# Kernel optimization log

Hardware: AMD Instinct MI355X
Metric: run time of the kernel (lower is better)

## Reference

```python
import jax, jax.numpy as jnp
import numpy as np

B, N_BOX, N_THING, ROI = 2, 32, 4, 28
H, W = 768, 704
N_STUFF = 6
N_CLS = N_STUFF + N_THING  # 10
NEG = -100.0


def setup_inputs() -> dict:
    key = jax.random.key(0)
    k1, k2, k3, k4 = jax.random.split(key, 4)
    sem_logits = jax.random.normal(k1, (B, N_CLS, H, W), jnp.float32)
    roi_msk_logits = jax.random.normal(k2, (B, N_BOX, N_THING, ROI, ROI), jnp.float32)
    cls = jax.random.randint(k3, (B, N_BOX), 0, N_THING, jnp.int32)
    u = jax.random.uniform(k4, (B, N_BOX, 4), jnp.float32)
    y0 = u[..., 0] * (H - 80.0)
    x0 = u[..., 1] * (W - 80.0)
    y1 = jnp.minimum(y0 + 32.0 + u[..., 2] * (H / 3.0), H - 1.0)
    x1 = jnp.minimum(x0 + 32.0 + u[..., 3] * (W / 3.0), W - 1.0)
    bbx = jnp.stack([y0, x0, y1, x1], axis=-1)  # (y_min, x_min, y_max, x_max)
    img_size = jnp.array([H, W], jnp.int32)
    return {"sem_logits": sem_logits, "roi_msk_logits": roi_msk_logits,
            "bbx": bbx, "cls": cls, "img_size": img_size}


def _bilinear_paste(msk, bbx, img_size, Hs, Ws):
    # msk: [B,N,R,R]; per-box bilinear resize (align_corners=False) to (h,w) and paste
    # into a [B,N,Hs,Ws] canvas filled with -100, clipped to the image.
    R = msk.shape[-1]
    ref = jnp.floor(bbx).astype(jnp.int32)  # torch .long()/int() truncation (boxes >= 0)
    y0, x0, y1, x1 = ref[..., 0], ref[..., 1], ref[..., 2], ref[..., 3]
    h = jnp.maximum(y1 - y0 + 1, 1).astype(jnp.float32)
    w = jnp.maximum(x1 - x0 + 1, 1).astype(jnp.float32)
    yy = jnp.arange(Hs, dtype=jnp.float32)[None, None, :]          # [1,1,H]
    sy = jnp.clip((yy - y0[..., None] + 0.5) * (R / h)[..., None] - 0.5, 0.0, R - 1.0)
    ylo = jnp.floor(sy).astype(jnp.int32)
    yhi = jnp.minimum(ylo + 1, R - 1)
    wy = sy - ylo                                                   # [B,N,H]
    xx = jnp.arange(Ws, dtype=jnp.float32)[None, None, :]
    sx = jnp.clip((xx - x0[..., None] + 0.5) * (R / w)[..., None] - 0.5, 0.0, R - 1.0)
    xlo = jnp.floor(sx).astype(jnp.int32)
    xhi = jnp.minimum(xlo + 1, R - 1)
    wx = sx - xlo                                                   # [B,N,W]
    rows = (jnp.take_along_axis(msk, ylo[..., None], axis=2) * (1.0 - wy[..., None])
            + jnp.take_along_axis(msk, yhi[..., None], axis=2) * wy[..., None])  # [B,N,H,R]
    up = (jnp.take_along_axis(rows, xlo[:, :, None, :], axis=3) * (1.0 - wx[:, :, None, :])
          + jnp.take_along_axis(rows, xhi[:, :, None, :], axis=3) * wx[:, :, None, :])  # [B,N,H,W]
    yi = jnp.arange(Hs, dtype=jnp.int32)[None, None, :]
    xi = jnp.arange(Ws, dtype=jnp.int32)[None, None, :]
    in_y = (yi >= jnp.maximum(y0, 0)[..., None]) & (yi < jnp.minimum(y1 + 1, img_size[0])[..., None])
    in_x = (xi >= jnp.maximum(x0, 0)[..., None]) & (xi < jnp.minimum(x1 + 1, img_size[1])[..., None])
    inside = in_y[..., :, None] & in_x[..., None, :]
    return jnp.where(inside, up, NEG)


def _fused_logits(sem_logits, roi_msk_logits, bbx, cls, img_size):
    Bs, _, Hs, Ws = sem_logits.shape
    Nb = cls.shape[1]
    # gather per-box mask logits for its predicted thing class: [B,N,R,R]
    msk = roi_msk_logits[jnp.arange(Bs)[:, None], jnp.arange(Nb)[None, :], cls]
    po_mask = _bilinear_paste(msk, bbx, img_size, Hs, Ws)          # [B,N,H,W]
    # semantic-logit crops per box (po_sem_stride = 1)
    iy0 = jnp.floor(bbx[..., 0]).astype(jnp.int32)
    ix0 = jnp.floor(bbx[..., 1]).astype(jnp.int32)
    iy1 = (jnp.round(bbx[..., 2]) + 1.0).astype(jnp.int32)
    ix1 = (jnp.round(bbx[..., 3]) + 1.0).astype(jnp.int32)
    yi = jnp.arange(Hs, dtype=jnp.int32)[None, None, :]
    xi = jnp.arange(Ws, dtype=jnp.int32)[None, None, :]
    in2 = (((yi >= iy0[..., None]) & (yi < iy1[..., None]))[..., :, None]
           & ((xi >= ix0[..., None]) & (xi < ix1[..., None]))[..., None, :])
    sem_sel = sem_logits[:, N_STUFF:][jnp.arange(Bs)[:, None], cls]  # [B,N,H,W]
    po_inst = jnp.where(in2, sem_sel, NEG)
    combined = (jax.nn.sigmoid(po_inst) + jax.nn.sigmoid(po_mask)) * (po_inst + po_mask)
    return jnp.concatenate([sem_logits[:, :N_STUFF], combined], axis=1)  # [B,6+N,H,W]


def _label_single(pp, sp, cl):
    # pp: panoptic argmax [H,W]; sp: semantic argmax [H,W]; cl: [N] thing classes
    Nb = cl.shape[0]
    is_inst = pp >= N_STUFF
    nmap = jnp.clip(pp - N_STUFF, 0, Nb - 1)
    # joint histogram counts[n, c] = #pixels with po_pred == 6+n and sem_pred == c
    key = jnp.where(is_inst, (pp - N_STUFF) * N_CLS + sp, Nb * N_CLS)
    counts = jnp.zeros(Nb * N_CLS + 1, jnp.int32).at[key.ravel()].add(1)[:Nb * N_CLS].reshape(Nb, N_CLS)
    present = counts.sum(1) > 0
    idx = jnp.cumsum(present.astype(jnp.int32)) - 1  # enumeration order of torch.unique ids
    maj = jnp.argmax(counts, axis=1).astype(jnp.int32)  # ties -> smallest class (matches unique+argmax)
    frac = counts.max(1).astype(jnp.float32) / jnp.maximum(counts.sum(1), 1).astype(jnp.float32)
    thing = cl.astype(jnp.int32) + N_STUFF
    match = maj == thing
    to_stuff = (~match) & (frac >= 0.5) & (maj < N_STUFF)
    sem_val = jnp.where(to_stuff, maj, thing)
    inst_val = jnp.where(to_stuff, -1, idx)
    po_sem = jnp.where(is_inst, sem_val[nmap], pp)
    po_inst = jnp.where(is_inst, inst_val[nmap], -1)
    # po_min_stuff_area = 0 (default) -> stuff-area filter is a no-op
    sh = jnp.zeros(N_STUFF + 1, jnp.int32).at[jnp.where(po_sem < N_STUFF, po_sem, N_STUFF).ravel()].add(1)[:N_STUFF]
    s_present = sh > 0
    s_rank = jnp.cumsum(s_present.astype(jnp.int32)) - 1
    n_stuff = s_present.astype(jnp.int32).sum()
    ih = jnp.zeros(Nb + 1, jnp.int32).at[jnp.where(po_inst >= 0, po_inst, Nb).ravel()].add(1)[:Nb]
    i_present = ih > 0
    i_rank = jnp.cumsum(i_present.astype(jnp.int32)) - 1
    seam = jnp.where((po_inst < 0) & (po_sem < N_STUFF),
                     1 + s_rank[jnp.clip(po_sem, 0, N_STUFF - 1)], 0)
    seam = jnp.where(po_inst >= 0, 1 + n_stuff + i_rank[jnp.clip(po_inst, 0, Nb - 1)], seam)
    L = 1 + N_STUFF + Nb  # fixed-size padded po_cls (torch version is variable-length)
    cls_out = jnp.full(L, 255, jnp.int32)
    cls_out = cls_out.at[jnp.where(s_present, 1 + s_rank, L)].set(
        jnp.arange(N_STUFF, dtype=jnp.int32), mode='drop')
    inst_sem = jnp.full(Nb, 255, jnp.int32).at[
        jnp.where(present & (~to_stuff), idx, Nb)].set(sem_val.astype(jnp.int32), mode='drop')
    cls_out = cls_out.at[jnp.where(i_present, 1 + n_stuff + i_rank, L)].set(inst_sem, mode='drop')
    return seam.astype(jnp.int32), cls_out, jnp.zeros(L, jnp.int32)


def reference(sem_logits, roi_msk_logits, bbx, cls, img_size):
    logits = _fused_logits(sem_logits, roi_msk_logits, bbx, cls, img_size)
    po_pred = jnp.argmax(logits, axis=1)        # softmax is monotone -> argmax of logits
    sem_pred = jnp.argmax(sem_logits, axis=1)
    seam, po_cls, po_iscrowd = jax.vmap(_label_single)(po_pred, sem_pred, cls)
    Bs, Hs, Ws = seam.shape
    return seam.reshape(Bs * Hs, Ws), po_cls.reshape(-1), po_iscrowd.reshape(-1)
```

## Files before the change

kernel.cpp:

```cpp
#include <hip/hip_runtime.h>
#include <math.h>

#define NSTUFF 6
#define NCLS   10
#define NBOX   32
#define NTHING 4
#define RR     28
#define HH     768
#define WW     704
#define NPIX   (HH * WW)
#define BB     2
#define LL     (1 + NSTUFF + NBOX)
#define NEGV   (-100.0f)

#define TW 64
#define TH 8
#define TILES_X (WW / TW)
#define TILES_Y (HH / TH)
#define NTILES  (TILES_X * TILES_Y)

__device__ __forceinline__ float sigmoidf_(float x) {
    return 1.0f / (1.0f + expf(-x));
}

__global__ __launch_bounds__(256) void k_fuse(
    const float* __restrict__ sem,
    const float* __restrict__ roi,
    const float* __restrict__ bbx,
    const int*   __restrict__ cls,
    int*         __restrict__ pred,
    int*         __restrict__ counts,
    int*         __restrict__ stuffh)
{
    const int b = blockIdx.y;
    __shared__ int   sh_y0[NBOX], sh_x0[NBOX], sh_yme[NBOX], sh_xme[NBOX];
    __shared__ int   sh_yie[NBOX], sh_xie[NBOX], sh_moff[NBOX], sh_cls[NBOX];
    __shared__ float sh_y0f[NBOX], sh_x0f[NBOX], sh_sy[NBOX], sh_sx[NBOX];
    __shared__ int   sh_list[NBOX];
    __shared__ int   sh_nbox;
    __shared__ int   sh_cnt[NBOX * NCLS + NSTUFF];

    const int t = threadIdx.x;
    const int tile = blockIdx.x;
    const int tx0 = (tile % TILES_X) * TW;
    const int ty0 = (tile / TILES_X) * TH;

    const int x  = tx0 + (t & (TW - 1));
    const int yA = ty0 + (t >> 6);
    const int yB = yA + 4;
    const int pA = yA * WW + x;
    const int pB = yB * WW + x;

    const float* semb = sem + (size_t)b * NCLS * NPIX;
    float s0[NCLS], s1[NCLS];
    #pragma unroll
    for (int c = 0; c < NCLS; ++c) s0[c] = semb[(size_t)c * NPIX + pA];
    #pragma unroll
    for (int c = 0; c < NCLS; ++c) s1[c] = semb[(size_t)c * NPIX + pB];

    for (int i = t; i < NBOX * NCLS + NSTUFF; i += blockDim.x) sh_cnt[i] = 0;

    if (t < 64) {
        bool flag = false;
        if (t < NBOX) {
            const float* bbp = bbx + ((size_t)b * NBOX + t) * 4;
            float y0f = bbp[0], x0f = bbp[1], y1f = bbp[2], x1f = bbp[3];
            int y0 = (int)floorf(y0f), x0 = (int)floorf(x0f);
            int y1 = (int)floorf(y1f), x1 = (int)floorf(x1f);
            int yme = min(y1 + 1, HH), xme = min(x1 + 1, WW);
            int yie = (int)rintf(y1f) + 1, xie = (int)rintf(x1f) + 1;
            sh_y0[t] = y0;  sh_x0[t] = x0;
            sh_yme[t] = yme; sh_xme[t] = xme;
            sh_yie[t] = yie; sh_xie[t] = xie;
            sh_y0f[t] = (float)y0; sh_x0f[t] = (float)x0;
            float hh = (float)max(y1 - y0 + 1, 1);
            float ww = (float)max(x1 - x0 + 1, 1);
            sh_sy[t] = 28.0f / hh;  sh_sx[t] = 28.0f / ww;
            int c = cls[b * NBOX + t];
            sh_cls[t] = c;
            sh_moff[t] = (((b * NBOX + t) * NTHING) + c) * (RR * RR);
            int uy = max(yme, yie), ux = max(xme, xie);
            flag = (y0 < ty0 + TH) && (uy > ty0) && (x0 < tx0 + TW) && (ux > tx0);
        }
        unsigned long long m = __ballot(flag);
        if (flag) {
            int pos = __popcll(m & (((unsigned long long)1 << t) - 1ull));
            sh_list[pos] = t;
        }
        if (t == 0) sh_nbox = __popcll(m);
    }
    __syncthreads();

    const int nb = sh_nbox;

    auto doPix = [&](const float* s, int y, int x_, float yf, float xf,
                     int& bi_o, int& sp_o) {
        float sb = s[0]; int sp = 0;
        #pragma unroll
        for (int c = 1; c < NCLS; ++c) if (s[c] > sb) { sb = s[c]; sp = c; }

        float bv = s[0]; int bi = 0;
        #pragma unroll
        for (int c = 1; c < NSTUFF; ++c) if (s[c] > bv) { bv = s[c]; bi = c; }

        int prev = -1;
        for (int j = 0; j < nb; ++j) {
            const int n = sh_list[j];
            if (n > prev + 1 && bv < 0.0f) { bv = -0.0f; bi = NSTUFF + prev + 1; }
            const bool in_m = (y >= max(sh_y0[n], 0)) & (y < sh_yme[n]) &
                              (x_ >= max(sh_x0[n], 0)) & (x_ < sh_xme[n]);
            const bool in_i = (y >= sh_y0[n]) & (y < sh_yie[n]) &
                              (x_ >= sh_x0[n]) & (x_ < sh_xie[n]);
            float v;
            if (in_m | in_i) {
                float pm = NEGV;
                if (in_m) {
                    float sy = __fsub_rn(__fmul_rn(__fadd_rn(__fsub_rn(yf, sh_y0f[n]), 0.5f), sh_sy[n]), 0.5f);
                    sy = fminf(fmaxf(sy, 0.0f), 27.0f);
                    int ylo = (int)sy;
                    int yhi = min(ylo + 1, RR - 1);
                    float wy = __fsub_rn(sy, (float)ylo);
                    float sx = __fsub_rn(__fmul_rn(__fadd_rn(__fsub_rn(xf, sh_x0f[n]), 0.5f), sh_sx[n]), 0.5f);
                    sx = fminf(fmaxf(sx, 0.0f), 27.0f);
                    int xlo = (int)sx;
                    int xhi = min(xlo + 1, RR - 1);
                    float wx = __fsub_rn(sx, (float)xlo);
                    const float* m = roi + sh_moff[n];
                    float m00 = m[ylo * RR + xlo], m01 = m[ylo * RR + xhi];
                    float m10 = m[yhi * RR + xlo], m11 = m[yhi * RR + xhi];
                    float omy = __fsub_rn(1.0f, wy), omx = __fsub_rn(1.0f, wx);
                    float rl = __fadd_rn(__fmul_rn(m00, omy), __fmul_rn(m10, wy));
                    float rh = __fadd_rn(__fmul_rn(m01, omy), __fmul_rn(m11, wy));
                    pm = __fadd_rn(__fmul_rn(rl, omx), __fmul_rn(rh, wx));
                }
                float pi = NEGV;
                if (in_i) {
                    int c = sh_cls[n];
                    pi = (c == 0) ? s[6] : (c == 1) ? s[7] : (c == 2) ? s[8] : s[9];
                }
                v = __fmul_rn(__fadd_rn(sigmoidf_(pi), sigmoidf_(pm)), __fadd_rn(pi, pm));
            } else {
                v = -0.0f;
            }
            if (v > bv) { bv = v; bi = NSTUFF + n; }
            prev = n;
        }
        if (prev < NBOX - 1 && bv < 0.0f) { bi = NSTUFF + prev + 1; }
        bi_o = bi; sp_o = sp;
    };

    int biA, spA, biB, spB;
    doPix(s0, yA, x, (float)yA, (float)x, biA, spA);
    doPix(s1, yB, x, (float)yB, (float)x, biB, spB);

    pred[(size_t)b * NPIX + pA] = biA;
    pred[(size_t)b * NPIX + pB] = biB;

    const int lane = t & 63;
    #pragma unroll
    for (int s = 0; s < NSTUFF; ++s) {
        unsigned long long mA = __ballot(biA == s);
        unsigned long long mB = __ballot(biB == s);
        int c = __popcll(mA) + __popcll(mB);
        if (lane == 0 && c) atomicAdd(&sh_cnt[NBOX * NCLS + s], c);
    }
    if (biA >= NSTUFF) atomicAdd(&sh_cnt[(biA - NSTUFF) * NCLS + spA], 1);
    if (biB >= NSTUFF) atomicAdd(&sh_cnt[(biB - NSTUFF) * NCLS + spB], 1);

    __syncthreads();
    for (int i = t; i < NBOX * NCLS + NSTUFF; i += blockDim.x) {
        int v = sh_cnt[i];
        if (v) {
            if (i < NBOX * NCLS) atomicAdd(&counts[b * NBOX * NCLS + i], v);
            else                 atomicAdd(&stuffh[b * NSTUFF + (i - NBOX * NCLS)], v);
        }
    }
}

__global__ __launch_bounds__(64) void k_label(
    const int* __restrict__ counts,
    const int* __restrict__ stuffh,
    const int* __restrict__ cls,
    int*       __restrict__ out,
    int*       __restrict__ lut)
{
    const int b = blockIdx.x;
    const int t = threadIdx.x;
    __shared__ int l_sh[NSTUFF];
    __shared__ int l_ih[NBOX];
    __shared__ int l_isem[NBOX];
    __shared__ int l_co[LL];

    if (t < NSTUFF) l_sh[t] = stuffh[b * NSTUFF + t];
    if (t < NBOX)  { l_ih[t] = 0; l_isem[t] = 255; }
    if (t < LL)      l_co[t] = 255;

    int  ssum = 0, mj = 0, semv = 0, idx = -1;
    bool pres = false, ts = false;
    if (t < NBOX) {
        const int* C = counts + ((size_t)b * NBOX + t) * NCLS;
        int c[NCLS];
        #pragma unroll
        for (int i = 0; i < NCLS; ++i) c[i] = C[i];
        int m = c[0]; mj = 0; ssum = c[0];
        #pragma unroll
        for (int i = 1; i < NCLS; ++i) {
            ssum += c[i];
            if (c[i] > m) { m = c[i]; mj = i; }
        }
        pres = ssum > 0;
        int thing = cls[b * NBOX + t] + NSTUFF;
        ts = pres && (mj != thing) && (2 * m >= ssum) && (mj < NSTUFF);
        semv = ts ? mj : thing;
    }
    unsigned long long pm = __ballot(pres);
    idx = __popcll(pm & (((unsigned long long)2 << t) - 1ull)) - 1;
    __syncthreads();

    if (t < NBOX && pres &&  ts) atomicAdd(&l_sh[mj], ssum);
    if (t < NBOX && pres && !ts) { atomicAdd(&l_ih[idx], ssum); l_isem[idx] = semv; }
    __syncthreads();

    bool spres = (t < NSTUFF) && (l_sh[t] > 0);
    unsigned long long sm = __ballot(spres);
    const int nst = __popcll(sm);
    bool ipres = (t < NBOX) && (l_ih[t] > 0);
    unsigned long long im = __ballot(ipres);

    auto srank = [&](int c) { return __popcll(sm & (((unsigned long long)2 << c) - 1ull)) - 1; };
    auto irank = [&](int j) { return __popcll(im & (((unsigned long long)2 << j) - 1ull)) - 1; };

    int* lb = lut + b * (NSTUFF + NBOX);
    if (t < NSTUFF) lb[t] = 1 + srank(t);
    if (t < NBOX) {
        int q = idx < 0 ? 0 : idx;
        lb[NSTUFF + t] = ts ? (1 + srank(mj)) : (1 + nst + irank(q));
    }

    if (spres) l_co[1 + srank(t)] = t;
    if (ipres) l_co[1 + nst + irank(t)] = l_isem[t];
    __syncthreads();

    int* ocls = out + (size_t)BB * NPIX + b * LL;
    int* ocrd = out + (size_t)BB * NPIX + BB * LL + b * LL;
    if (t < LL) { ocls[t] = l_co[t]; ocrd[t] = 0; }
}

__global__ __launch_bounds__(256) void k_seam(int* __restrict__ out,
                                              const int* __restrict__ lut)
{
    __shared__ int slut[BB * (NSTUFF + NBOX)];
    for (int i = threadIdx.x; i < BB * (NSTUFF + NBOX); i += blockDim.x)
        slut[i] = lut[i];
    __syncthreads();
    const size_t gid = (size_t)blockIdx.x * blockDim.x + threadIdx.x;
    int4 v = ((const int4*)out)[gid];
    const int base = (gid >= (size_t)(NPIX / 4)) ? (NSTUFF + NBOX) : 0;
    v.x = slut[base + v.x];
    v.y = slut[base + v.y];
    v.z = slut[base + v.z];
    v.w = slut[base + v.w];
    ((int4*)out)[gid] = v;
}

extern "C" void kernel_launch(void* const* d_in, const int* in_sizes, int n_in,
                              void* d_out, int out_size, void* d_ws, size_t ws_size,
                              hipStream_t stream) {
    (void)in_sizes; (void)n_in; (void)out_size; (void)ws_size;
    const float* sem = (const float*)d_in[0];
    const float* roi = (const float*)d_in[1];
    const float* bbx = (const float*)d_in[2];
    const int*   cls = (const int*)d_in[3];
    int* out = (int*)d_out;

    int* counts = (int*)d_ws;
    int* stuffh = counts + BB * NBOX * NCLS;
    int* lut    = stuffh + BB * NSTUFF;

    hipMemsetAsync(d_ws, 0, (BB * NBOX * NCLS + BB * NSTUFF) * sizeof(int), stream);

    dim3 g1(NTILES, BB);
    k_fuse<<<g1, 256, 0, stream>>>(sem, roi, bbx, cls, out, counts, stuffh);
    k_label<<<BB, 64, 0, stream>>>(counts, stuffh, cls, out, lut);
    k_seam<<<(BB * NPIX / 4) / 256, 256, 0, stream>>>(out, lut);
}
```

Before: 118.8 us.

## Vectorize per-thread pixels and fuse label computation into relabel pass

In the fused-logits kernel, each thread now handles four horizontally adjacent pixels through float4 loads of the semantic logits and an int4 store of predictions. Tiles are taller, so there are half as many blocks and fewer global histogram atomics. The separate label kernel is merged into the relabel kernel: every block recomputes the small LUT from the histograms in shared memory, which removes one launch and the LUT round trip through global memory. In exchange, each relabel block repeats the label logic, and each thread now holds four pixels' worth of registers, which may lower occupancy.

```diff
diff --git a/kernel.cpp b/kernel.cpp
--- a/kernel.cpp
+++ b/kernel.cpp
@@ -14,10 +14,11 @@
 #define NEGV   (-100.0f)
 
 #define TW 64
-#define TH 8
+#define TH 16
 #define TILES_X (WW / TW)
 #define TILES_Y (HH / TH)
 #define NTILES  (TILES_X * TILES_Y)
+#define NHIST   (NBOX * NCLS + NSTUFF)
 
 __device__ __forceinline__ float sigmoidf_(float x) {
     return 1.0f / (1.0f + expf(-x));
@@ -38,27 +39,24 @@
     __shared__ float sh_y0f[NBOX], sh_x0f[NBOX], sh_sy[NBOX], sh_sx[NBOX];
     __shared__ int   sh_list[NBOX];
     __shared__ int   sh_nbox;
-    __shared__ int   sh_cnt[NBOX * NCLS + NSTUFF];
+    __shared__ int   sh_cnt[NHIST];
 
     const int t = threadIdx.x;
     const int tile = blockIdx.x;
     const int tx0 = (tile % TILES_X) * TW;
     const int ty0 = (tile / TILES_X) * TH;
 
-    const int x  = tx0 + (t & (TW - 1));
-    const int yA = ty0 + (t >> 6);
-    const int yB = yA + 4;
-    const int pA = yA * WW + x;
-    const int pB = yB * WW + x;
+    const int xq = tx0 + (t & 15) * 4;
+    const int y  = ty0 + (t >> 4);
+    const int p  = y * WW + xq;
 
     const float* semb = sem + (size_t)b * NCLS * NPIX;
-    float s0[NCLS], s1[NCLS];
-    #pragma unroll
-    for (int c = 0; c < NCLS; ++c) s0[c] = semb[(size_t)c * NPIX + pA];
-    #pragma unroll
-    for (int c = 0; c < NCLS; ++c) s1[c] = semb[(size_t)c * NPIX + pB];
-
-    for (int i = t; i < NBOX * NCLS + NSTUFF; i += blockDim.x) sh_cnt[i] = 0;
+    float4 s4[NCLS];
+    #pragma unroll
+    for (int c = 0; c < NCLS; ++c)
+        s4[c] = *(const float4*)(semb + (size_t)c * NPIX + p);
+
+    for (int i = t; i < NHIST; i += 256) sh_cnt[i] = 0;
 
     if (t < 64) {
         bool flag = false;
@@ -93,8 +91,8 @@
 
     const int nb = sh_nbox;
 
-    auto doPix = [&](const float* s, int y, int x_, float yf, float xf,
-                     int& bi_o, int& sp_o) {
+    auto doPix = [&](const float* s, int y_, int x_, int& bi_o, int& sp_o) {
+        const float yf = (float)y_, xf = (float)x_;
         float sb = s[0]; int sp = 0;
         #pragma unroll
         for (int c = 1; c < NCLS; ++c) if (s[c] > sb) { sb = s[c]; sp = c; }
@@ -107,9 +105,9 @@
         for (int j = 0; j < nb; ++j) {
             const int n = sh_list[j];
             if (n > prev + 1 && bv < 0.0f) { bv = -0.0f; bi = NSTUFF + prev + 1; }
-            const bool in_m = (y >= max(sh_y0[n], 0)) & (y < sh_yme[n]) &
+            const bool in_m = (y_ >= max(sh_y0[n], 0)) & (y_ < sh_yme[n]) &
                               (x_ >= max(sh_x0[n], 0)) & (x_ < sh_xme[n]);
-            const bool in_i = (y >= sh_y0[n]) & (y < sh_yie[n]) &
+            const bool in_i = (y_ >= sh_y0[n]) & (y_ < sh_yie[n]) &
                               (x_ >= sh_x0[n]) & (x_ < sh_xie[n]);
             float v;
             if (in_m | in_i) {
@@ -149,26 +147,32 @@
         bi_o = bi; sp_o = sp;
     };
 
-    int biA, spA, biB, spB;
-    doPix(s0, yA, x, (float)yA, (float)x, biA, spA);
-    doPix(s1, yB, x, (float)yB, (float)x, biB, spB);
-
-    pred[(size_t)b * NPIX + pA] = biA;
-    pred[(size_t)b * NPIX + pB] = biB;
+    int bis[4], sps[4];
+    #pragma unroll
+    for (int j = 0; j < 4; ++j) {
+        float s[NCLS];
+        #pragma unroll
+        for (int c = 0; c < NCLS; ++c) s[c] = ((const float*)&s4[c])[j];
+        doPix(s, y, xq + j, bis[j], sps[j]);
+    }
+
+    int4 pv; pv.x = bis[0]; pv.y = bis[1]; pv.z = bis[2]; pv.w = bis[3];
+    *(int4*)(pred + (size_t)b * NPIX + p) = pv;
 
     const int lane = t & 63;
     #pragma unroll
     for (int s = 0; s < NSTUFF; ++s) {
-        unsigned long long mA = __ballot(biA == s);
-        unsigned long long mB = __ballot(biB == s);
-        int c = __popcll(mA) + __popcll(mB);
+        int c = 0;
+        #pragma unroll
+        for (int j = 0; j < 4; ++j) c += __popcll(__ballot(bis[j] == s));
         if (lane == 0 && c) atomicAdd(&sh_cnt[NBOX * NCLS + s], c);
     }
-    if (biA >= NSTUFF) atomicAdd(&sh_cnt[(biA - NSTUFF) * NCLS + spA], 1);
-    if (biB >= NSTUFF) atomicAdd(&sh_cnt[(biB - NSTUFF) * NCLS + spB], 1);
-
-    __syncthreads();
-    for (int i = t; i < NBOX * NCLS + NSTUFF; i += blockDim.x) {
+    #pragma unroll
+    for (int j = 0; j < 4; ++j)
+        if (bis[j] >= NSTUFF) atomicAdd(&sh_cnt[(bis[j] - NSTUFF) * NCLS + sps[j]], 1);
+
+    __syncthreads();
+    for (int i = t; i < NHIST; i += 256) {
         int v = sh_cnt[i];
         if (v) {
             if (i < NBOX * NCLS) atomicAdd(&counts[b * NBOX * NCLS + i], v);
@@ -177,90 +181,86 @@
     }
 }
 
-__global__ __launch_bounds__(64) void k_label(
+__global__ __launch_bounds__(256) void k_relabel(
     const int* __restrict__ counts,
     const int* __restrict__ stuffh,
     const int* __restrict__ cls,
-    int*       __restrict__ out,
-    int*       __restrict__ lut)
+    int*       __restrict__ out)
 {
-    const int b = blockIdx.x;
+    const int b = blockIdx.y;
     const int t = threadIdx.x;
+    __shared__ int slut[NSTUFF + NBOX];
     __shared__ int l_sh[NSTUFF];
     __shared__ int l_ih[NBOX];
     __shared__ int l_isem[NBOX];
     __shared__ int l_co[LL];
 
-    if (t < NSTUFF) l_sh[t] = stuffh[b * NSTUFF + t];
-    if (t < NBOX)  { l_ih[t] = 0; l_isem[t] = 255; }
-    if (t < LL)      l_co[t] = 255;
-
     int  ssum = 0, mj = 0, semv = 0, idx = -1;
     bool pres = false, ts = false;
-    if (t < NBOX) {
-        const int* C = counts + ((size_t)b * NBOX + t) * NCLS;
-        int c[NCLS];
-        #pragma unroll
-        for (int i = 0; i < NCLS; ++i) c[i] = C[i];
-        int m = c[0]; mj = 0; ssum = c[0];
-        #pragma unroll
-        for (int i = 1; i < NCLS; ++i) {
-            ssum += c[i];
-            if (c[i] > m) { m = c[i]; mj = i; }
-        }
-        pres = ssum > 0;
-        int thing = cls[b * NBOX + t] + NSTUFF;
-        ts = pres && (mj != thing) && (2 * m >= ssum) && (mj < NSTUFF);
-        semv = ts ? mj : thing;
-    }
-    unsigned long long pm = __ballot(pres);
-    idx = __popcll(pm & (((unsigned long long)2 << t) - 1ull)) - 1;
-    __syncthreads();
-
-    if (t < NBOX && pres &&  ts) atomicAdd(&l_sh[mj], ssum);
-    if (t < NBOX && pres && !ts) { atomicAdd(&l_ih[idx], ssum); l_isem[idx] = semv; }
-    __syncthreads();
-
-    bool spres = (t < NSTUFF) && (l_sh[t] > 0);
-    unsigned long long sm = __ballot(spres);
-    const int nst = __popcll(sm);
-    bool ipres = (t < NBOX) && (l_ih[t] > 0);
-    unsigned long long im = __ballot(ipres);
-
-    auto srank = [&](int c) { return __popcll(sm & (((unsigned long long)2 << c) - 1ull)) - 1; };
-    auto irank = [&](int j) { return __popcll(im & (((unsigned long long)2 << j) - 1ull)) - 1; };
-
-    int* lb = lut + b * (NSTUFF + NBOX);
-    if (t < NSTUFF) lb[t] = 1 + srank(t);
-    if (t < NBOX) {
-        int q = idx < 0 ? 0 : idx;
-        lb[NSTUFF + t] = ts ? (1 + srank(mj)) : (1 + nst + irank(q));
-    }
-
-    if (spres) l_co[1 + srank(t)] = t;
-    if (ipres) l_co[1 + nst + irank(t)] = l_isem[t];
-    __syncthreads();
-
-    int* ocls = out + (size_t)BB * NPIX + b * LL;
-    int* ocrd = out + (size_t)BB * NPIX + BB * LL + b * LL;
-    if (t < LL) { ocls[t] = l_co[t]; ocrd[t] = 0; }
-}
-
-__global__ __launch_bounds__(256) void k_seam(int* __restrict__ out,
-                                              const int* __restrict__ lut)
-{
-    __shared__ int slut[BB * (NSTUFF + NBOX)];
-    for (int i = threadIdx.x; i < BB * (NSTUFF + NBOX); i += blockDim.x)
-        slut[i] = lut[i];
-    __syncthreads();
-    const size_t gid = (size_t)blockIdx.x * blockDim.x + threadIdx.x;
-    int4 v = ((const int4*)out)[gid];
-    const int base = (gid >= (size_t)(NPIX / 4)) ? (NSTUFF + NBOX) : 0;
-    v.x = slut[base + v.x];
-    v.y = slut[base + v.y];
-    v.z = slut[base + v.z];
-    v.w = slut[base + v.w];
-    ((int4*)out)[gid] = v;
+
+    if (t < 64) {
+        if (t < NSTUFF) l_sh[t] = stuffh[b * NSTUFF + t];
+        if (t < NBOX)  { l_ih[t] = 0; l_isem[t] = 255; }
+        if (t < LL)      l_co[t] = 255;
+
+        if (t < NBOX) {
+            const int* C = counts + ((size_t)b * NBOX + t) * NCLS;
+            int c[NCLS];
+            #pragma unroll
+            for (int i = 0; i < NCLS; ++i) c[i] = C[i];
+            int m = c[0]; mj = 0; ssum = c[0];
+            #pragma unroll
+            for (int i = 1; i < NCLS; ++i) {
+                ssum += c[i];
+                if (c[i] > m) { m = c[i]; mj = i; }
+            }
+            pres = ssum > 0;
+            int thing = cls[b * NBOX + t] + NSTUFF;
+            ts = pres && (mj != thing) && (2 * m >= ssum) && (mj < NSTUFF);
+            semv = ts ? mj : thing;
+        }
+        unsigned long long pm = __ballot(pres);
+        idx = __popcll(pm & (((unsigned long long)2 << t) - 1ull)) - 1;
+
+        if (t < NBOX && pres &&  ts) atomicAdd(&l_sh[mj], ssum);
+        if (t < NBOX && pres && !ts) { atomicAdd(&l_ih[idx], ssum); l_isem[idx] = semv; }
+    }
+    __syncthreads();
+
+    if (t < 64) {
+        bool spres = (t < NSTUFF) && (l_sh[t] > 0);
+        unsigned long long sm = __ballot(spres);
+        const int nst = __popcll(sm);
+        bool ipres = (t < NBOX) && (l_ih[t] > 0);
+        unsigned long long im = __ballot(ipres);
+
+        auto srank = [&](int c) { return __popcll(sm & (((unsigned long long)2 << c) - 1ull)) - 1; };
+        auto irank = [&](int j) { return __popcll(im & (((unsigned long long)2 << j) - 1ull)) - 1; };
+
+        if (t < NSTUFF) slut[t] = 1 + srank(t);
+        if (t < NBOX) {
+            int q = idx < 0 ? 0 : idx;
+            slut[NSTUFF + t] = ts ? (1 + srank(mj)) : (1 + nst + irank(q));
+        }
+        if (spres) l_co[1 + srank(t)] = t;
+        if (ipres) l_co[1 + nst + irank(t)] = l_isem[t];
+    }
+    __syncthreads();
+
+    const size_t gi = (size_t)b * (NPIX / 4) + (size_t)blockIdx.x * 256 + t;
+    int4 v = ((const int4*)out)[gi];
+    v.x = slut[v.x];
+    v.y = slut[v.y];
+    v.z = slut[v.z];
+    v.w = slut[v.w];
+    ((int4*)out)[gi] = v;
+
+    if (blockIdx.x == 0 && t < LL) {
+        int* ocls = out + (size_t)BB * NPIX + b * LL;
+        int* ocrd = out + (size_t)BB * NPIX + BB * LL + b * LL;
+        ocls[t] = l_co[t];
+        ocrd[t] = 0;
+    }
 }
 
 extern "C" void kernel_launch(void* const* d_in, const int* in_sizes, int n_in,
@@ -275,12 +275,11 @@
 
     int* counts = (int*)d_ws;
     int* stuffh = counts + BB * NBOX * NCLS;
-    int* lut    = stuffh + BB * NSTUFF;
 
     hipMemsetAsync(d_ws, 0, (BB * NBOX * NCLS + BB * NSTUFF) * sizeof(int), stream);
 
     dim3 g1(NTILES, BB);
     k_fuse<<<g1, 256, 0, stream>>>(sem, roi, bbx, cls, out, counts, stuffh);
-    k_label<<<BB, 64, 0, stream>>>(counts, stuffh, cls, out, lut);
-    k_seam<<<(BB * NPIX / 4) / 256, 256, 0, stream>>>(out, lut);
-}
+    dim3 g2(NPIX / 1024, BB);
+    k_relabel<<<g2, 256, 0, stream>>>(counts, stuffh, cls, out);
+}
```

Measured after the change: 110.0 us. 1.08x faster.
